# Kernel tuning notes

Hardware: AMD Instinct MI355X
Metric: run time of the kernel (lower is better)

Reference implementation:

```python
import jax, jax.numpy as jnp
import numpy as np

EMB = 128
HEADS = 4
OUT = EMB // HEADS
NL = 50000
NR = 50000
E = 800000


def setup_inputs() -> dict:
    key = jax.random.key(0)
    ks = jax.random.split(key, 20)
    s = 0.05  # param init scale
    f32 = jnp.float32
    return {
        "left_features": jax.random.normal(ks[0], (NL, EMB), f32),
        "edge_indices": jax.random.randint(ks[1], (2, E), 0, NL),  # NL == NR
        "edge_features": jax.random.normal(ks[2], (E, EMB), f32),
        "right_features": jax.random.normal(ks[3], (NR, EMB), f32),
        # GATv2Conv params
        "W_l": jax.random.normal(ks[4], (EMB, HEADS * OUT), f32) * s,
        "b_l": jnp.zeros((HEADS * OUT,), f32),
        "W_r": jax.random.normal(ks[5], (EMB, HEADS * OUT), f32) * s,
        "b_r": jnp.zeros((HEADS * OUT,), f32),
        "W_e": jax.random.normal(ks[6], (EMB, HEADS * OUT), f32) * s,
        "att": jax.random.normal(ks[7], (HEADS, OUT), f32) * s,
        "b_conv": jnp.zeros((HEADS * OUT,), f32),
        # LayerNorm
        "ln_g": jnp.ones((EMB,), f32),
        "ln_b": jnp.zeros((EMB,), f32),
        # output MLP
        "W1": jax.random.normal(ks[8], (2 * EMB, EMB), f32) * s,
        "b1": jnp.zeros((EMB,), f32),
        "W2": jax.random.normal(ks[9], (EMB, EMB), f32) * s,
        "b2": jnp.zeros((EMB,), f32),
    }


def reference(left_features, edge_indices, edge_features, right_features,
              W_l, b_l, W_r, b_r, W_e, att, b_conv, ln_g, ln_b,
              W1, b1, W2, b2):
    H, O = att.shape
    n_right = right_features.shape[0]
    src = edge_indices[0]
    dst = edge_indices[1]

    # linear projections (GATv2: separate lin_l for src, lin_r for dst, lin_edge no bias)
    x_l = (left_features @ W_l + b_l).reshape(-1, H, O)   # [NL,H,O]
    x_r = (right_features @ W_r + b_r).reshape(-1, H, O)  # [NR,H,O]
    e = (edge_features @ W_e).reshape(-1, H, O)           # [E,H,O]

    # per-edge GATv2 attention logits
    z = jax.nn.leaky_relu(x_l[src] + x_r[dst] + e, 0.2)   # [E,H,O]
    logits = jnp.einsum('eho,ho->eh', z, att)             # [E,H]

    # segment softmax over destination nodes
    m = jax.ops.segment_max(logits, dst, num_segments=n_right)
    m = jnp.where(jnp.isfinite(m), m, 0.0)  # guard empty segments
    ex = jnp.exp(logits - m[dst])
    den = jax.ops.segment_sum(ex, dst, num_segments=n_right)
    alpha = ex / (den[dst] + 1e-16)                       # [E,H]

    # message = transformed src feature weighted by alpha, scatter-add to dst
    msg = jax.ops.segment_sum(x_l[src] * alpha[:, :, None], dst,
                              num_segments=n_right)       # [NR,H,O]
    msg = msg.reshape(n_right, H * O) + b_conv            # concat heads + bias

    # LayerNorm
    mu = jnp.mean(msg, axis=-1, keepdims=True)
    var = jnp.mean(jnp.square(msg - mu), axis=-1, keepdims=True)
    msg = (msg - mu) * jax.lax.rsqrt(var + 1e-5) * ln_g + ln_b

    # out MLP on [msg, right_features]
    h = jnp.concatenate([msg, right_features], axis=-1)
    h = jax.nn.relu(h @ W1 + b1)
    return h @ W2 + b2
```

## Files before the change

kernel.cpp:

```cpp
#include <hip/hip_runtime.h>
#include <math.h>

#define EMB 128

typedef __bf16 bf16x8 __attribute__((ext_vector_type(8)));
typedef float f32x4 __attribute__((ext_vector_type(4)));


__device__ __forceinline__ int incl_scan_256(int v, int* lds) {
    int tid = threadIdx.x;
    lds[tid] = v;
    __syncthreads();
    #pragma unroll
    for (int off = 1; off < 256; off <<= 1) {
        int t = (tid >= off) ? lds[tid - off] : 0;
        __syncthreads();
        lds[tid] += t;
        __syncthreads();
    }
    return lds[tid];
}

__global__ void pack_w_kernel(const float* __restrict__ W, __bf16* __restrict__ pack, int K) {
    const int ksteps = K >> 5;
    const int nchunk = 8 * ksteps * 64;
    for (int idx = blockIdx.x * 256 + threadIdx.x; idx < nchunk; idx += 256 * gridDim.x) {
        int l = idx & 63;
        int s = (idx >> 6) % ksteps;
        int t = (idx >> 6) / ksteps;
        #pragma unroll
        for (int j = 0; j < 8; ++j) {
            int k = s * 32 + ((l >> 4) * 8) + j;
            int n = t * 16 + (l & 15);
            pack[(size_t)idx * 8 + j] = (__bf16)W[(size_t)k * EMB + n];
        }
    }
}

template<int KSTEPS>
__global__ __launch_bounds__(256) void proj_mfma(
    const float* __restrict__ X0, const float* __restrict__ X1,
    const __bf16* __restrict__ wpack, const float* __restrict__ bias,
    float* __restrict__ Y, int M, int relu)
{
    __shared__ __attribute__((aligned(16))) __bf16 Wl[KSTEPS * 8 * 64 * 8];
    const int tid = threadIdx.x;
    #pragma unroll
    for (int i = tid; i < KSTEPS * 512; i += 256)
        ((float4*)Wl)[i] = ((const float4*)wpack)[i];
    __syncthreads();

    const int l = tid & 63, wv = tid >> 6;
    const int q = l >> 4, c = l & 15;
    const int rbase = blockIdx.x * 64 + wv * 16;

    int arow = rbase + c; if (arow >= M) arow = M - 1;
    const float* Ap0 = X0 + (size_t)arow * EMB + q * 8;
    const float* Ap1 = (KSTEPS == 8) ? (X1 + (size_t)arow * EMB + q * 8) : Ap0;

    f32x4 acc[8];
    #pragma unroll
    for (int t = 0; t < 8; ++t) acc[t] = (f32x4){0.f, 0.f, 0.f, 0.f};

    #pragma unroll
    for (int s = 0; s < KSTEPS; ++s) {
        const float* bp = (s < 4) ? Ap0 : Ap1;
        const int ss = (s < 4) ? s : s - 4;
        float4 a0 = *(const float4*)(bp + ss * 32);
        float4 a1 = *(const float4*)(bp + ss * 32 + 4);
        bf16x8 af;
        af[0] = (__bf16)a0.x; af[1] = (__bf16)a0.y; af[2] = (__bf16)a0.z; af[3] = (__bf16)a0.w;
        af[4] = (__bf16)a1.x; af[5] = (__bf16)a1.y; af[6] = (__bf16)a1.z; af[7] = (__bf16)a1.w;
        #pragma unroll
        for (int t = 0; t < 8; ++t) {
            bf16x8 bf = *reinterpret_cast<const bf16x8*>(&Wl[((size_t)(t * KSTEPS + s) * 64 + l) * 8]);
            acc[t] = __builtin_amdgcn_mfma_f32_16x16x32_bf16(af, bf, acc[t], 0, 0, 0);
        }
    }

    const int r0 = rbase + q * 4;
    #pragma unroll
    for (int t = 0; t < 8; ++t) {
        const int col = t * 16 + c;
        const float b = bias ? bias[col] : 0.f;
        #pragma unroll
        for (int i = 0; i < 4; ++i) {
            const int r = r0 + i;
            if (r < M) {
                float v = acc[t][i] + b;
                if (relu) v = fmaxf(v, 0.f);
                Y[(size_t)r * EMB + col] = v;
            }
        }
    }
}

__global__ __launch_bounds__(256) void edge_kernel(
    const float* __restrict__ EF, const __bf16* __restrict__ wpack,
    const float* __restrict__ xl, const float* __restrict__ xr,
    const int* __restrict__ src, const int* __restrict__ dst,
    const float* __restrict__ att, float* __restrict__ exb, int En)
{
    __shared__ __attribute__((aligned(16))) __bf16 Wl[EMB * EMB];
    const int tid = threadIdx.x;
    {
        float4* d4 = (float4*)Wl;
        const float4* s4 = (const float4*)wpack;
        #pragma unroll
        for (int i = 0; i < 8; ++i) d4[tid + 256 * i] = s4[tid + 256 * i];
    }
    __syncthreads();

    const int l = tid & 63, wv = tid >> 6;
    const int q = l >> 4, c = l & 15;
    const int ebase = blockIdx.x * 64 + wv * 16;

    f32x4 acc[8];
    #pragma unroll
    for (int t = 0; t < 8; ++t) acc[t] = (f32x4){0.f, 0.f, 0.f, 0.f};

    int arow = ebase + c; if (arow >= En) arow = En - 1;
    const float* Ap = EF + (size_t)arow * EMB + q * 8;

    #pragma unroll
    for (int s = 0; s < 4; ++s) {
        float4 a0 = *(const float4*)(Ap + s * 32);
        float4 a1 = *(const float4*)(Ap + s * 32 + 4);
        bf16x8 af;
        af[0] = (__bf16)a0.x; af[1] = (__bf16)a0.y; af[2] = (__bf16)a0.z; af[3] = (__bf16)a0.w;
        af[4] = (__bf16)a1.x; af[5] = (__bf16)a1.y; af[6] = (__bf16)a1.z; af[7] = (__bf16)a1.w;
        #pragma unroll
        for (int t = 0; t < 8; ++t) {
            bf16x8 bf = *reinterpret_cast<const bf16x8*>(&Wl[((size_t)(t * 4 + s) * 64 + l) * 8]);
            acc[t] = __builtin_amdgcn_mfma_f32_16x16x32_bf16(af, bf, acc[t], 0, 0, 0);
        }
    }

    float attv[8];
    #pragma unroll
    for (int t = 0; t < 8; ++t) attv[t] = att[t * 16 + c];

    float v[4][4];
    const int e0 = ebase + q * 4;
    #pragma unroll
    for (int i = 0; i < 4; ++i) {
        int ei = e0 + i; if (ei >= En) ei = En - 1;
        const int se = src[ei], de = dst[ei];
        const float* xls = xl + (size_t)se * EMB;
        const float* xrs = xr + (size_t)de * EMB;
        float ph[4] = {0.f, 0.f, 0.f, 0.f};
        #pragma unroll
        for (int t = 0; t < 8; ++t) {
            int col = t * 16 + c;
            float z = acc[t][i] + xls[col] + xrs[col];
            z = (z > 0.f) ? z : 0.2f * z;
            ph[t >> 1] += z * attv[t];
        }
        #pragma unroll
        for (int h = 0; h < 4; ++h) v[i][h] = ph[h];
    }

    #pragma unroll
    for (int m = 1; m < 16; m <<= 1) {
        #pragma unroll
        for (int i = 0; i < 4; ++i)
            #pragma unroll
            for (int h = 0; h < 4; ++h)
                v[i][h] += __shfl_xor(v[i][h], m);
    }

    const int si = c >> 2, sh = c & 3;
    float val = v[0][0];
    #pragma unroll
    for (int i = 0; i < 4; ++i)
        #pragma unroll
        for (int h = 0; h < 4; ++h)
            if (si == i && sh == h) val = v[i][h];
    const int ew = e0 + si;
    if (ew < En) exb[(size_t)ew * 4 + sh] = expf(val);
}

__global__ void hist_kernel(const int* __restrict__ dst, int* __restrict__ counts, int En) {
    int i = blockIdx.x * 256 + threadIdx.x;
    if (i < En) atomicAdd(&counts[dst[i]], 1);
}

__global__ void scan1_kernel(const int* __restrict__ counts, int* __restrict__ bsum, int N) {
    __shared__ int red[4];
    int i = blockIdx.x * 256 + threadIdx.x;
    int v = (i < N) ? counts[i] : 0;
    #pragma unroll
    for (int m = 1; m < 64; m <<= 1) v += __shfl_xor(v, m);
    if ((threadIdx.x & 63) == 0) red[threadIdx.x >> 6] = v;
    __syncthreads();
    if (threadIdx.x == 0) bsum[blockIdx.x] = red[0] + red[1] + red[2] + red[3];
}

__global__ void scan2_kernel(int* __restrict__ bsum, int* __restrict__ boff, int nb,
                             int* __restrict__ offs, int NRtot, int Etot) {
    __shared__ int lds[256];
    int tid = threadIdx.x;
    int v = (tid < nb) ? bsum[tid] : 0;
    int incl = incl_scan_256(v, lds);
    if (tid < nb) boff[tid] = incl - v;
    if (tid == 0) offs[NRtot] = Etot;
}

__global__ void scan3_kernel(const int* __restrict__ counts, const int* __restrict__ boff,
                             int* __restrict__ offs, int* __restrict__ cursor, int N) {
    __shared__ int lds[256];
    int tid = threadIdx.x;
    int i = blockIdx.x * 256 + tid;
    int v = (i < N) ? counts[i] : 0;
    int incl = incl_scan_256(v, lds);
    int excl = incl - v + boff[blockIdx.x];
    if (i < N) { offs[i] = excl; cursor[i] = excl; }
}

__global__ void scatter_kernel(const int* __restrict__ dst, int* __restrict__ cursor,
                               int* __restrict__ csr, int En) {
    int i = blockIdx.x * 256 + threadIdx.x;
    if (i < En) { int p = atomicAdd(&cursor[dst[i]], 1); csr[p] = i; }
}

__global__ __launch_bounds__(128) void msg_ln_kernel(
    const float* __restrict__ xl, const float* __restrict__ exb,
    const int* __restrict__ csr, const int* __restrict__ offs,
    const int* __restrict__ src, const float* __restrict__ bconv,
    const float* __restrict__ ln_g, const float* __restrict__ ln_b,
    float* __restrict__ msg)
{
    const int d = blockIdx.x;
    const int tid = threadIdx.x;
    const int h = tid >> 5;
    const int beg = offs[d], end = offs[d + 1];
    float acc = 0.f, den = 0.f;
    for (int i = beg; i < end; ++i) {
        int e = csr[i];
        float exv = exb[(size_t)e * 4 + h];
        int s = src[e];
        acc += exv * xl[(size_t)s * EMB + tid];
        den += exv;
    }
    float m = acc / (den + 1e-16f) + bconv[tid];

    __shared__ float red[2];
    float s1 = m;
    #pragma unroll
    for (int mk = 1; mk < 64; mk <<= 1) s1 += __shfl_xor(s1, mk);
    if ((tid & 63) == 0) red[tid >> 6] = s1;
    __syncthreads();
    float mu = (red[0] + red[1]) * (1.f / EMB);
    __syncthreads();
    float c = m - mu;
    float s2 = c * c;
    #pragma unroll
    for (int mk = 1; mk < 64; mk <<= 1) s2 += __shfl_xor(s2, mk);
    if ((tid & 63) == 0) red[tid >> 6] = s2;
    __syncthreads();
    float var = (red[0] + red[1]) * (1.f / EMB);
    float y = c * (1.f / sqrtf(var + 1e-5f)) * ln_g[tid] + ln_b[tid];
    msg[(size_t)d * EMB + tid] = y;
}

extern "C" void kernel_launch(void* const* d_in, const int* in_sizes, int n_in,
                              void* d_out, int out_size, void* d_ws, size_t ws_size,
                              hipStream_t stream) {
    const float* left  = (const float*)d_in[0];
    const int*   eidx  = (const int*)d_in[1];
    const float* ef    = (const float*)d_in[2];
    const float* right = (const float*)d_in[3];
    const float* W_l   = (const float*)d_in[4];
    const float* b_l   = (const float*)d_in[5];
    const float* W_r   = (const float*)d_in[6];
    const float* b_r   = (const float*)d_in[7];
    const float* W_e   = (const float*)d_in[8];
    const float* att   = (const float*)d_in[9];
    const float* bconv = (const float*)d_in[10];
    const float* ln_g  = (const float*)d_in[11];
    const float* ln_b  = (const float*)d_in[12];
    const float* W1    = (const float*)d_in[13];
    const float* b1    = (const float*)d_in[14];
    const float* W2    = (const float*)d_in[15];
    const float* b2    = (const float*)d_in[16];

    const int NLn = in_sizes[0] / EMB;
    const int En  = in_sizes[1] / 2;
    const int NRn = in_sizes[3] / EMB;
    const int* src  = eidx;
    const int* dstp = eidx + En;

    __bf16* we_pack = (__bf16*)d_ws;
    __bf16* wl_pack = we_pack + 16384;
    __bf16* wr_pack = wl_pack + 16384;
    __bf16* w1_pack = wr_pack + 16384;
    __bf16* w2_pack = w1_pack + 32768;
    float* fws = (float*)d_ws + 49152;
    size_t off = 0;
    float* x_l = fws + off; off += (size_t)NLn * EMB;
    float* x_r = fws + off; off += (size_t)NRn * EMB;
    float* exb = fws + off; off += (size_t)En * 4;
    float* msg = fws + off; off += (size_t)NRn * EMB;
    int* counts = (int*)(fws + off);
    int* offs   = counts + NRn;
    int* cursor = offs + NRn + 1;
    int* bsum   = cursor + NRn;
    int* boff   = bsum + 256;
    int* csr    = boff + 256;

    const int nb = (NRn + 255) / 256;
    const int gP_L = (NLn + 63) / 64;
    const int gP_R = (NRn + 63) / 64;
    const int gE64 = (En + 63) / 64;
    const int gE256 = (En + 255) / 256;

    hipMemsetAsync(counts, 0, (size_t)NRn * sizeof(int), stream);

    pack_w_kernel<<<8, 256, 0, stream>>>(W_e, we_pack, 128);
    pack_w_kernel<<<8, 256, 0, stream>>>(W_l, wl_pack, 128);
    pack_w_kernel<<<8, 256, 0, stream>>>(W_r, wr_pack, 128);
    pack_w_kernel<<<16, 256, 0, stream>>>(W1, w1_pack, 256);
    pack_w_kernel<<<8, 256, 0, stream>>>(W2, w2_pack, 128);

    proj_mfma<4><<<gP_L, 256, 0, stream>>>(left,  nullptr, wl_pack, b_l, x_l, NLn, 0);
    proj_mfma<4><<<gP_R, 256, 0, stream>>>(right, nullptr, wr_pack, b_r, x_r, NRn, 0);

    hist_kernel<<<gE256, 256, 0, stream>>>(dstp, counts, En);
    scan1_kernel<<<nb, 256, 0, stream>>>(counts, bsum, NRn);
    scan2_kernel<<<1, 256, 0, stream>>>(bsum, boff, nb, offs, NRn, En);
    scan3_kernel<<<nb, 256, 0, stream>>>(counts, boff, offs, cursor, NRn);
    scatter_kernel<<<gE256, 256, 0, stream>>>(dstp, cursor, csr, En);

    edge_kernel<<<gE64, 256, 0, stream>>>(ef, we_pack, x_l, x_r, src, dstp, att, exb, En);

    msg_ln_kernel<<<NRn, 128, 0, stream>>>(x_l, exb, csr, offs, src, bconv, ln_g, ln_b, msg);

    proj_mfma<8><<<gP_R, 256, 0, stream>>>(msg, right, w1_pack, b1, x_r, NRn, 1);
    proj_mfma<4><<<gP_R, 256, 0, stream>>>(x_r, nullptr, w2_pack, b2, (float*)d_out, NRn, 0);
}
```

Before: 979.4 us.

## Store edge weights in CSR order and fuse pack/projection launches

The scatter pass now records each edge's CSR position and writes a destination-sorted copy of the source indices. The edge kernel writes its exp logits directly at that sorted position, so the message kernel reads exb and src contiguously instead of indirecting through csr. The five weight-pack launches are merged into one kernel, and the left/right projections run in a single dual launch. The message loop is unrolled by four to keep more gathers in flight, and index and att loads are issued before the shared-memory barrier. The cost is an extra pos array plus scattered writes of exb from the edge kernel.

```diff
diff --git a/kernel.cpp b/kernel.cpp
--- a/kernel.cpp
+++ b/kernel.cpp
@@ -21,18 +21,75 @@
     return lds[tid];
 }
 
-__global__ void pack_w_kernel(const float* __restrict__ W, __bf16* __restrict__ pack, int K) {
+__global__ void pack_all_kernel(
+    const float* __restrict__ W_e, const float* __restrict__ W_l,
+    const float* __restrict__ W_r, const float* __restrict__ W1,
+    const float* __restrict__ W2,
+    __bf16* __restrict__ we, __bf16* __restrict__ wl, __bf16* __restrict__ wr,
+    __bf16* __restrict__ w1, __bf16* __restrict__ w2)
+{
+    int idx = blockIdx.x * 256 + threadIdx.x;
+    const float* W; __bf16* P; int K; int base;
+    if (idx < 2048)       { W = W_e; P = we; K = 128; base = 0; }
+    else if (idx < 4096)  { W = W_l; P = wl; K = 128; base = 2048; }
+    else if (idx < 6144)  { W = W_r; P = wr; K = 128; base = 4096; }
+    else if (idx < 10240) { W = W1;  P = w1; K = 256; base = 6144; }
+    else                  { W = W2;  P = w2; K = 128; base = 10240; }
+    idx -= base;
     const int ksteps = K >> 5;
-    const int nchunk = 8 * ksteps * 64;
-    for (int idx = blockIdx.x * 256 + threadIdx.x; idx < nchunk; idx += 256 * gridDim.x) {
-        int l = idx & 63;
-        int s = (idx >> 6) % ksteps;
-        int t = (idx >> 6) / ksteps;
-        #pragma unroll
-        for (int j = 0; j < 8; ++j) {
-            int k = s * 32 + ((l >> 4) * 8) + j;
-            int n = t * 16 + (l & 15);
-            pack[(size_t)idx * 8 + j] = (__bf16)W[(size_t)k * EMB + n];
+    const int l = idx & 63;
+    const int s = (idx >> 6) % ksteps;
+    const int t = (idx >> 6) / ksteps;
+    #pragma unroll
+    for (int j = 0; j < 8; ++j) {
+        int k = s * 32 + ((l >> 4) * 8) + j;
+        int n = t * 16 + (l & 15);
+        P[(size_t)idx * 8 + j] = (__bf16)W[(size_t)k * EMB + n];
+    }
+}
+
+__device__ __forceinline__ void proj4_compute(
+    const __bf16* Wl, const float* __restrict__ X, const float* __restrict__ bias,
+    float* __restrict__ Y, int M, int relu, int blk, int tid)
+{
+    const int l = tid & 63, wv = tid >> 6;
+    const int q = l >> 4, c = l & 15;
+    const int rbase = blk * 64 + wv * 16;
+
+    int arow = rbase + c; if (arow >= M) arow = M - 1;
+    const float* Ap = X + (size_t)arow * EMB + q * 8;
+
+    f32x4 acc[8];
+    #pragma unroll
+    for (int t = 0; t < 8; ++t) acc[t] = (f32x4){0.f, 0.f, 0.f, 0.f};
+
+    #pragma unroll
+    for (int s = 0; s < 4; ++s) {
+        float4 a0 = *(const float4*)(Ap + s * 32);
+        float4 a1 = *(const float4*)(Ap + s * 32 + 4);
+        bf16x8 af;
+        af[0] = (__bf16)a0.x; af[1] = (__bf16)a0.y; af[2] = (__bf16)a0.z; af[3] = (__bf16)a0.w;
+        af[4] = (__bf16)a1.x; af[5] = (__bf16)a1.y; af[6] = (__bf16)a1.z; af[7] = (__bf16)a1.w;
+        #pragma unroll
+        for (int t = 0; t < 8; ++t) {
+            bf16x8 bf = *reinterpret_cast<const bf16x8*>(&Wl[((size_t)(t * 4 + s) * 64 + l) * 8]);
+            acc[t] = __builtin_amdgcn_mfma_f32_16x16x32_bf16(af, bf, acc[t], 0, 0, 0);
+        }
+    }
+
+    const int r0 = rbase + q * 4;
+    #pragma unroll
+    for (int t = 0; t < 8; ++t) {
+        const int col = t * 16 + c;
+        const float b = bias ? bias[col] : 0.f;
+        #pragma unroll
+        for (int i = 0; i < 4; ++i) {
+            const int r = r0 + i;
+            if (r < M) {
+                float v = acc[t][i] + b;
+                if (relu) v = fmaxf(v, 0.f);
+                Y[(size_t)r * EMB + col] = v;
+            }
         }
     }
 }
@@ -95,10 +152,29 @@
     }
 }
 
+__global__ __launch_bounds__(256) void proj_dual(
+    const float* __restrict__ XA, const __bf16* __restrict__ wpA,
+    const float* __restrict__ bA, float* __restrict__ YA, int MA, int gA,
+    const float* __restrict__ XB, const __bf16* __restrict__ wpB,
+    const float* __restrict__ bB, float* __restrict__ YB, int MB)
+{
+    __shared__ __attribute__((aligned(16))) __bf16 Wl[4 * 8 * 64 * 8];
+    const int tid = threadIdx.x;
+    const bool second = (blockIdx.x >= gA);
+    const __bf16* wp = second ? wpB : wpA;
+    #pragma unroll
+    for (int i = tid; i < 2048; i += 256)
+        ((float4*)Wl)[i] = ((const float4*)wp)[i];
+    __syncthreads();
+    if (second) proj4_compute(Wl, XB, bB, YB, MB, 0, blockIdx.x - gA, tid);
+    else        proj4_compute(Wl, XA, bA, YA, MA, 0, blockIdx.x, tid);
+}
+
 __global__ __launch_bounds__(256) void edge_kernel(
     const float* __restrict__ EF, const __bf16* __restrict__ wpack,
     const float* __restrict__ xl, const float* __restrict__ xr,
     const int* __restrict__ src, const int* __restrict__ dst,
+    const int* __restrict__ pos,
     const float* __restrict__ att, float* __restrict__ exb, int En)
 {
     __shared__ __attribute__((aligned(16))) __bf16 Wl[EMB * EMB];
@@ -109,11 +185,23 @@
         #pragma unroll
         for (int i = 0; i < 8; ++i) d4[tid + 256 * i] = s4[tid + 256 * i];
     }
-    __syncthreads();
 
     const int l = tid & 63, wv = tid >> 6;
     const int q = l >> 4, c = l & 15;
     const int ebase = blockIdx.x * 64 + wv * 16;
+    const int e0 = ebase + q * 4;
+
+    int ses[4], des[4];
+    #pragma unroll
+    for (int i = 0; i < 4; ++i) {
+        int ei = e0 + i; if (ei >= En) ei = En - 1;
+        ses[i] = src[ei]; des[i] = dst[ei];
+    }
+    float attv[8];
+    #pragma unroll
+    for (int t = 0; t < 8; ++t) attv[t] = att[t * 16 + c];
+
+    __syncthreads();
 
     f32x4 acc[8];
     #pragma unroll
@@ -136,18 +224,11 @@
         }
     }
 
-    float attv[8];
-    #pragma unroll
-    for (int t = 0; t < 8; ++t) attv[t] = att[t * 16 + c];
-
     float v[4][4];
-    const int e0 = ebase + q * 4;
     #pragma unroll
     for (int i = 0; i < 4; ++i) {
-        int ei = e0 + i; if (ei >= En) ei = En - 1;
-        const int se = src[ei], de = dst[ei];
-        const float* xls = xl + (size_t)se * EMB;
-        const float* xrs = xr + (size_t)de * EMB;
+        const float* xls = xl + (size_t)ses[i] * EMB;
+        const float* xrs = xr + (size_t)des[i] * EMB;
         float ph[4] = {0.f, 0.f, 0.f, 0.f};
         #pragma unroll
         for (int t = 0; t < 8; ++t) {
@@ -177,7 +258,10 @@
         for (int h = 0; h < 4; ++h)
             if (si == i && sh == h) val = v[i][h];
     const int ew = e0 + si;
-    if (ew < En) exb[(size_t)ew * 4 + sh] = expf(val);
+    if (ew < En) {
+        int p = pos[ew];
+        exb[(size_t)p * 4 + sh] = expf(val);
+    }
 }
 
 __global__ void hist_kernel(const int* __restrict__ dst, int* __restrict__ counts, int En) {
@@ -217,16 +301,21 @@
     if (i < N) { offs[i] = excl; cursor[i] = excl; }
 }
 
-__global__ void scatter_kernel(const int* __restrict__ dst, int* __restrict__ cursor,
-                               int* __restrict__ csr, int En) {
+__global__ void scatter_kernel(const int* __restrict__ dst, const int* __restrict__ srcv,
+                               int* __restrict__ cursor, int* __restrict__ pos,
+                               int* __restrict__ src_sorted, int En) {
     int i = blockIdx.x * 256 + threadIdx.x;
-    if (i < En) { int p = atomicAdd(&cursor[dst[i]], 1); csr[p] = i; }
+    if (i < En) {
+        int p = atomicAdd(&cursor[dst[i]], 1);
+        pos[i] = p;
+        src_sorted[p] = srcv[i];
+    }
 }
 
 __global__ __launch_bounds__(128) void msg_ln_kernel(
     const float* __restrict__ xl, const float* __restrict__ exb,
-    const int* __restrict__ csr, const int* __restrict__ offs,
-    const int* __restrict__ src, const float* __restrict__ bconv,
+    const int* __restrict__ src_sorted, const int* __restrict__ offs,
+    const float* __restrict__ bconv,
     const float* __restrict__ ln_g, const float* __restrict__ ln_b,
     float* __restrict__ msg)
 {
@@ -234,15 +323,33 @@
     const int tid = threadIdx.x;
     const int h = tid >> 5;
     const int beg = offs[d], end = offs[d + 1];
+    const float bc = bconv[tid], g = ln_g[tid], bb = ln_b[tid];
+
     float acc = 0.f, den = 0.f;
-    for (int i = beg; i < end; ++i) {
-        int e = csr[i];
-        float exv = exb[(size_t)e * 4 + h];
-        int s = src[e];
-        acc += exv * xl[(size_t)s * EMB + tid];
-        den += exv;
-    }
-    float m = acc / (den + 1e-16f) + bconv[tid];
+    int i = beg;
+    for (; i + 4 <= end; i += 4) {
+        int s0 = src_sorted[i + 0], s1 = src_sorted[i + 1];
+        int s2 = src_sorted[i + 2], s3 = src_sorted[i + 3];
+        float ev0 = exb[(size_t)(i + 0) * 4 + h];
+        float ev1 = exb[(size_t)(i + 1) * 4 + h];
+        float ev2 = exb[(size_t)(i + 2) * 4 + h];
+        float ev3 = exb[(size_t)(i + 3) * 4 + h];
+        float x0 = xl[(size_t)s0 * EMB + tid];
+        float x1 = xl[(size_t)s1 * EMB + tid];
+        float x2 = xl[(size_t)s2 * EMB + tid];
+        float x3 = xl[(size_t)s3 * EMB + tid];
+        acc += ev0 * x0; den += ev0;
+        acc += ev1 * x1; den += ev1;
+        acc += ev2 * x2; den += ev2;
+        acc += ev3 * x3; den += ev3;
+    }
+    for (; i < end; ++i) {
+        int s = src_sorted[i];
+        float ev = exb[(size_t)i * 4 + h];
+        acc += ev * xl[(size_t)s * EMB + tid];
+        den += ev;
+    }
+    float m = acc / (den + 1e-16f) + bc;
 
     __shared__ float red[2];
     float s1 = m;
@@ -252,14 +359,14 @@
     __syncthreads();
     float mu = (red[0] + red[1]) * (1.f / EMB);
     __syncthreads();
-    float c = m - mu;
-    float s2 = c * c;
+    float cm = m - mu;
+    float s2 = cm * cm;
     #pragma unroll
     for (int mk = 1; mk < 64; mk <<= 1) s2 += __shfl_xor(s2, mk);
     if ((tid & 63) == 0) red[tid >> 6] = s2;
     __syncthreads();
     float var = (red[0] + red[1]) * (1.f / EMB);
-    float y = c * (1.f / sqrtf(var + 1e-5f)) * ln_g[tid] + ln_b[tid];
+    float y = cm * (1.f / sqrtf(var + 1e-5f)) * g + bb;
     msg[(size_t)d * EMB + tid] = y;
 }
 
@@ -301,12 +408,13 @@
     float* x_r = fws + off; off += (size_t)NRn * EMB;
     float* exb = fws + off; off += (size_t)En * 4;
     float* msg = fws + off; off += (size_t)NRn * EMB;
-    int* counts = (int*)(fws + off);
-    int* offs   = counts + NRn;
-    int* cursor = offs + NRn + 1;
-    int* bsum   = cursor + NRn;
-    int* boff   = bsum + 256;
-    int* csr    = boff + 256;
+    int* counts     = (int*)(fws + off);
+    int* offs       = counts + NRn;
+    int* cursor     = offs + NRn + 1;
+    int* bsum       = cursor + NRn;
+    int* boff       = bsum + 256;
+    int* pos        = boff + 256;
+    int* src_sorted = pos + En;
 
     const int nb = (NRn + 255) / 256;
     const int gP_L = (NLn + 63) / 64;
@@ -316,24 +424,21 @@
 
     hipMemsetAsync(counts, 0, (size_t)NRn * sizeof(int), stream);
 
-    pack_w_kernel<<<8, 256, 0, stream>>>(W_e, we_pack, 128);
-    pack_w_kernel<<<8, 256, 0, stream>>>(W_l, wl_pack, 128);
-    pack_w_kernel<<<8, 256, 0, stream>>>(W_r, wr_pack, 128);
-    pack_w_kernel<<<16, 256, 0, stream>>>(W1, w1_pack, 256);
-    pack_w_kernel<<<8, 256, 0, stream>>>(W2, w2_pack, 128);
-
-    proj_mfma<4><<<gP_L, 256, 0, stream>>>(left,  nullptr, wl_pack, b_l, x_l, NLn, 0);
-    proj_mfma<4><<<gP_R, 256, 0, stream>>>(right, nullptr, wr_pack, b_r, x_r, NRn, 0);
+    pack_all_kernel<<<48, 256, 0, stream>>>(W_e, W_l, W_r, W1, W2,
+                                            we_pack, wl_pack, wr_pack, w1_pack, w2_pack);
+
+    proj_dual<<<gP_L + gP_R, 256, 0, stream>>>(left, wl_pack, b_l, x_l, NLn, gP_L,
+                                               right, wr_pack, b_r, x_r, NRn);
 
     hist_kernel<<<gE256, 256, 0, stream>>>(dstp, counts, En);
     scan1_kernel<<<nb, 256, 0, stream>>>(counts, bsum, NRn);
     scan2_kernel<<<1, 256, 0, stream>>>(bsum, boff, nb, offs, NRn, En);
     scan3_kernel<<<nb, 256, 0, stream>>>(counts, boff, offs, cursor, NRn);
-    scatter_kernel<<<gE256, 256, 0, stream>>>(dstp, cursor, csr, En);
-
-    edge_kernel<<<gE64, 256, 0, stream>>>(ef, we_pack, x_l, x_r, src, dstp, att, exb, En);
-
-    msg_ln_kernel<<<NRn, 128, 0, stream>>>(x_l, exb, csr, offs, src, bconv, ln_g, ln_b, msg);
+    scatter_kernel<<<gE256, 256, 0, stream>>>(dstp, src, cursor, pos, src_sorted, En);
+
+    edge_kernel<<<gE64, 256, 0, stream>>>(ef, we_pack, x_l, x_r, src, dstp, pos, att, exb, En);
+
+    msg_ln_kernel<<<NRn, 128, 0, stream>>>(x_l, exb, src_sorted, offs, bconv, ln_g, ln_b, msg);
 
     proj_mfma<8><<<gP_R, 256, 0, stream>>>(msg, right, w1_pack, b1, x_r, NRn, 1);
     proj_mfma<4><<<gP_R, 256, 0, stream>>>(x_r, nullptr, w2_pack, b2, (float*)d_out, NRn, 0);
```

Result: faster. 901.4 us (-8.0%).
